# Performance work log

Measured on AMD Instinct MI355X. Metric: run time of the kernel, lower is better.

Reference implementation:

```python
import jax, jax.numpy as jnp
import numpy as np

DIM = 1024
HEADS = 16
EPS = 1e-5


def layer_norm(x, gamma, beta):
    mu = jnp.mean(x, axis=-1, keepdims=True)
    var = jnp.mean(jnp.square(x - mu), axis=-1, keepdims=True)
    return (x - mu) * jax.lax.rsqrt(var + EPS) * gamma + beta


def setup_inputs() -> dict:
    key = jax.random.key(0)
    ks = jax.random.split(key, 9)
    B, Nq, Nk = 8, 1024, 1024
    s = 1.0 / np.sqrt(DIM)
    return {
        "x": jax.random.normal(ks[0], (B, Nq, DIM), jnp.float32),
        "context": jax.random.normal(ks[1], (B, Nk, DIM), jnp.float32),
        "relative_position_bias": jax.random.normal(ks[2], (HEADS, Nq, Nk), jnp.float32),
        "Wq": jax.random.normal(ks[3], (DIM, DIM), jnp.float32) * s,
        "Wk": jax.random.normal(ks[4], (DIM, DIM), jnp.float32) * s,
        "Wv": jax.random.normal(ks[5], (DIM, DIM), jnp.float32) * s,
        "Wo": jax.random.normal(ks[6], (DIM, DIM), jnp.float32) * s,
        "bo": jnp.zeros((DIM,), jnp.float32),
        "gamma": jnp.ones((DIM,), jnp.float32),
        "beta": jnp.zeros((DIM,), jnp.float32),
    }


def reference(x, context, relative_position_bias, Wq, Wk, Wv, Wo, bo, gamma, beta):
    h = HEADS
    d = DIM // h
    scale = d ** -0.5
    xn = layer_norm(x, gamma, beta)
    cn = layer_norm(context, gamma, beta)
    B, Nq, _ = x.shape
    Nk = context.shape[1]
    # b n (h d) -> b h n d
    q = (xn @ Wq).reshape(B, Nq, h, d).transpose(0, 2, 1, 3)
    k = (cn @ Wk).reshape(B, Nk, h, d).transpose(0, 2, 1, 3)
    v = (cn @ Wv).reshape(B, Nk, h, d).transpose(0, 2, 1, 3)
    scores = jnp.einsum('bhid,bhjd->bhij', q, k) * scale
    scores = scores + relative_position_bias[None]
    attn = jax.nn.softmax(scores, axis=-1)
    out = jnp.einsum('bhij,bhjd->bhid', attn, v)
    out = out.transpose(0, 2, 1, 3).reshape(B, Nq, h * d)
    return out @ Wo + bo
```

## Files before the change

### kernel.cpp

```cpp
#include <hip/hip_runtime.h>
#include <hip/hip_bf16.h>
#include <stdint.h>

#define DIM   1024
#define HEADS 16
#define HD    64
#define NB    8
#define NTOK  1024
#define MROWS (NB*NTOK)

#define LOG2E 1.4426950408889634f
#define SCL   (0.125f * LOG2E)

typedef __attribute__((ext_vector_type(8))) _Float16 f16x8;
typedef __attribute__((ext_vector_type(4))) _Float16 f16x4;
typedef __attribute__((ext_vector_type(4))) float    f32x4;

typedef unsigned int uint_as1 __attribute__((address_space(1)));
typedef unsigned int uint_as3 __attribute__((address_space(3)));

__device__ __forceinline__ void gload16(const void* g, void* l) {
    __builtin_amdgcn_global_load_lds((const uint_as1*)g, (uint_as3*)l, 16, 0, 0);
}

__device__ __forceinline__ unsigned pkrtz(float a, float b) {
    auto h = __builtin_amdgcn_cvt_pkrtz(a, b);
    return __builtin_bit_cast(unsigned, h);
}

#if __has_builtin(__builtin_amdgcn_permlane32_swap)
__device__ __forceinline__ void swap32(unsigned& a, unsigned& b) {
    auto r = __builtin_amdgcn_permlane32_swap(a, b, false, false);
    a = r[0]; b = r[1];
}
#else
__device__ __forceinline__ void swap32(unsigned& a, unsigned& b) {
    unsigned as = (unsigned)__shfl_xor((int)a, 32, 64);
    unsigned bs = (unsigned)__shfl_xor((int)b, 32, 64);
    bool lo = ((threadIdx.x & 63) < 32);
    unsigned na = lo ? a : bs, nb = lo ? as : b;
    a = na; b = nb;
}
#endif
#if __has_builtin(__builtin_amdgcn_permlane16_swap)
__device__ __forceinline__ void swap16(unsigned& a, unsigned& b) {
    auto r = __builtin_amdgcn_permlane16_swap(a, b, false, false);
    a = r[0]; b = r[1];
}
#else
__device__ __forceinline__ void swap16(unsigned& a, unsigned& b) {
    unsigned as = (unsigned)__shfl_xor((int)a, 16, 64);
    unsigned bs = (unsigned)__shfl_xor((int)b, 16, 64);
    bool ev = ((threadIdx.x & 16) == 0);
    unsigned na = ev ? a : bs, nb = ev ? as : b;
    a = na; b = nb;
}
#endif
__device__ __forceinline__ float redmax32(float x) {
    unsigned a = __builtin_bit_cast(unsigned, x), b = a;
    swap32(a, b);
    return fmaxf(__builtin_bit_cast(float, a), __builtin_bit_cast(float, b));
}
__device__ __forceinline__ float redmax16(float x) {
    unsigned a = __builtin_bit_cast(unsigned, x), b = a;
    swap16(a, b);
    return fmaxf(__builtin_bit_cast(float, a), __builtin_bit_cast(float, b));
}
__device__ __forceinline__ float redsum32(float x) {
    unsigned a = __builtin_bit_cast(unsigned, x), b = a;
    swap32(a, b);
    return __builtin_bit_cast(float, a) + __builtin_bit_cast(float, b);
}
__device__ __forceinline__ float redsum16(float x) {
    unsigned a = __builtin_bit_cast(unsigned, x), b = a;
    swap16(a, b);
    return __builtin_bit_cast(float, a) + __builtin_bit_cast(float, b);
}

__global__ __launch_bounds__(256) void ln_kernel(const float* __restrict__ x,
                                                 const float* __restrict__ ctx,
                                                 const float* __restrict__ gamma,
                                                 const float* __restrict__ beta,
                                                 _Float16* __restrict__ xn,
                                                 _Float16* __restrict__ cn) {
    int row = blockIdx.x;
    const float* src; _Float16* dst;
    if (row < MROWS) { src = x + (size_t)row * DIM;          dst = xn + (size_t)row * DIM; }
    else             { int r = row - MROWS;
                       src = ctx + (size_t)r * DIM;          dst = cn + (size_t)r * DIM; }
    int t = threadIdx.x;
    float4 v = *(const float4*)(src + t * 4);
    float s  = v.x + v.y + v.z + v.w;
    float s2 = v.x*v.x + v.y*v.y + v.z*v.z + v.w*v.w;
    #pragma unroll
    for (int o = 32; o; o >>= 1) { s += __shfl_xor(s, o, 64); s2 += __shfl_xor(s2, o, 64); }
    __shared__ float red[8];
    int w = t >> 6, l = t & 63;
    if (l == 0) { red[w] = s; red[4 + w] = s2; }
    __syncthreads();
    s  = red[0] + red[1] + red[2] + red[3];
    s2 = red[4] + red[5] + red[6] + red[7];
    float mu   = s * (1.0f / DIM);
    float rstd = rsqrtf(s2 * (1.0f / DIM) - mu * mu + 1e-5f);
    float4 g  = *(const float4*)(gamma + t * 4);
    float4 bb = *(const float4*)(beta  + t * 4);
    f16x4 o;
    o[0] = (_Float16)((v.x - mu) * rstd * g.x + bb.x);
    o[1] = (_Float16)((v.y - mu) * rstd * g.y + bb.y);
    o[2] = (_Float16)((v.z - mu) * rstd * g.z + bb.z);
    o[3] = (_Float16)((v.w - mu) * rstd * g.w + bb.w);
    *(f16x4*)(dst + t * 4) = o;
}

__global__ __launch_bounds__(256) void biasconv_kernel(const float* __restrict__ bias,
                                                       _Float16* __restrict__ bias2) {
    size_t i = ((size_t)blockIdx.x * 256 + threadIdx.x) * 8;
    float4 a = *(const float4*)(bias + i);
    float4 b = *(const float4*)(bias + i + 4);
    f16x8 o;
    o[0] = (_Float16)(a.x * LOG2E); o[1] = (_Float16)(a.y * LOG2E);
    o[2] = (_Float16)(a.z * LOG2E); o[3] = (_Float16)(a.w * LOG2E);
    o[4] = (_Float16)(b.x * LOG2E); o[5] = (_Float16)(b.y * LOG2E);
    o[6] = (_Float16)(b.z * LOG2E); o[7] = (_Float16)(b.w * LOG2E);
    *(f16x8*)(bias2 + i) = o;
}

__global__ __launch_bounds__(256) void wtrans_kernel(const float* __restrict__ Wq, const float* __restrict__ Wk,
                                                     const float* __restrict__ Wv, const float* __restrict__ Wo,
                                                     _Float16* __restrict__ Tq, _Float16* __restrict__ Tk,
                                                     _Float16* __restrict__ Tv, _Float16* __restrict__ To) {
    __shared__ float tile[32][33];
    int m = blockIdx.z;
    const float* W = (m == 0) ? Wq : (m == 1) ? Wk : (m == 2) ? Wv : Wo;
    _Float16*    T = (m == 0) ? Tq : (m == 1) ? Tk : (m == 2) ? Tv : To;
    int j0 = blockIdx.x * 32, k0 = blockIdx.y * 32;
    int tx = threadIdx.x, ty = threadIdx.y;
    #pragma unroll
    for (int i = 0; i < 4; i++) tile[ty + i*8][tx] = W[(size_t)(k0 + ty + i*8) * DIM + j0 + tx];
    __syncthreads();
    #pragma unroll
    for (int i = 0; i < 4; i++) T[(size_t)(j0 + ty + i*8) * DIM + k0 + tx] = (_Float16)tile[tx][ty + i*8];
}

template<int MODE>
__global__ __launch_bounds__(256) void gemm_bt(const _Float16* __restrict__ A,
                                               const _Float16* __restrict__ BT,
                                               void* __restrict__ Cout,
                                               const float* __restrict__ bias) {
    __shared__ _Float16 As[128 * 32];
    __shared__ _Float16 Bs[128 * 32];
    const int K = DIM;
    int m0 = blockIdx.x * 128, n0 = blockIdx.y * 128;
    int t = threadIdx.x, w = t >> 6, l = t & 63;
    int wr = w >> 1, wc = w & 1, ln = l & 15, qtr = l >> 4;
    f32x4 acc[4][4] = {};
    int srow = t >> 2, scol = (t & 3) * 8;
    const _Float16* Ag = A  + (size_t)(m0 + srow) * K + scol;
    const _Float16* Bg = BT + (size_t)(n0 + srow) * K + scol;
    _Float16* Al = &As[(w * 16) * 32];
    _Float16* Bl = &Bs[(w * 16) * 32];
    for (int kt = 0; kt < K; kt += 32) {
        gload16(Ag,                    Al);
        gload16(Ag + (size_t)64 * K,   Al + 64 * 32);
        gload16(Bg,                    Bl);
        gload16(Bg + (size_t)64 * K,   Bl + 64 * 32);
        Ag += 32; Bg += 32;
        __syncthreads();
        f16x8 af[4], bfr[4];
        #pragma unroll
        for (int r = 0; r < 4; r++) af[r]  = *(const f16x8*)&As[(wr * 64 + r * 16 + ln) * 32 + qtr * 8];
        #pragma unroll
        for (int c = 0; c < 4; c++) bfr[c] = *(const f16x8*)&Bs[(wc * 64 + c * 16 + ln) * 32 + qtr * 8];
        #pragma unroll
        for (int r = 0; r < 4; r++)
            #pragma unroll
            for (int c = 0; c < 4; c++)
                acc[r][c] = __builtin_amdgcn_mfma_f32_16x16x32_f16(af[r], bfr[c], acc[r][c], 0, 0, 0);
        __syncthreads();
    }
    #pragma unroll
    for (int r = 0; r < 4; r++)
        #pragma unroll
        for (int c = 0; c < 4; c++) {
            int gn = n0 + wc * 64 + c * 16 + ln;
            #pragma unroll
            for (int q = 0; q < 4; q++) {
                int gm = m0 + wr * 64 + r * 16 + qtr * 4 + q;
                float v = acc[r][c][q];
                if constexpr (MODE == 0) {
                    int b = gm >> 10, n = gm & 1023, h = gn >> 6, d = gn & 63;
                    ((_Float16*)Cout)[(((size_t)(b * HEADS + h) * NTOK + n) << 6) + d] = (_Float16)v;
                } else if constexpr (MODE == 2) {
                    int b = gm >> 10, n = gm & 1023, h = gn >> 6, d = gn & 63;
                    ((_Float16*)Cout)[(((size_t)(b * HEADS + h) * HD + d) << 10) + n] = (_Float16)v;
                } else {
                    ((float*)Cout)[(size_t)gm * DIM + gn] = v + bias[gn];
                }
            }
        }
}

__global__ __launch_bounds__(256) void attn_kernel(const _Float16* __restrict__ qb,
                                                   const _Float16* __restrict__ kb,
                                                   const _Float16* __restrict__ vt,
                                                   const _Float16* __restrict__ bias2,
                                                   _Float16* __restrict__ ao) {
    __shared__ _Float16 Kt[2][64 * 64];
    __shared__ _Float16 Vs[2][64 * 64];
    int bid = blockIdx.x;
    int id2 = (bid & 7) * 128 + (bid >> 3);
    int qt = id2 & 7, h = (id2 >> 3) & 15, b = id2 >> 7;
    int q0 = qt * 128;
    int t = threadIdx.x, w = t >> 6, l = t & 63, ln = l & 15, qtr = l >> 4;
    const _Float16* qbase = qb + (size_t)(b * HEADS + h) * NTOK * HD;
    const _Float16* kbase = kb + (size_t)(b * HEADS + h) * NTOK * HD;
    const _Float16* vbase = vt + (size_t)(b * HEADS + h) * HD * NTOK;
    const _Float16* bbase = bias2 + ((size_t)h * NTOK + q0 + w * 32) * NTOK;

    f16x8 qfr[2][2];
    #pragma unroll
    for (int qf = 0; qf < 2; qf++)
        #pragma unroll
        for (int ks = 0; ks < 2; ks++)
            qfr[qf][ks] = *(const f16x8*)&qbase[(size_t)(q0 + w*32 + qf*16 + ln) * HD + ks*32 + qtr*8];

#define STAGE(BUF, J0) do {                                                     \
        int rb_ = w * 16;                                                       \
        _Float16* kl_ = &Kt[BUF][rb_ * 64];                                     \
        _Float16* vl_ = &Vs[BUF][rb_ * 64];                                     \
        int r_ = rb_ + (l >> 3); int cg_ = (l & 7) ^ (r_ & 7);                  \
        gload16(kbase + (size_t)((J0) + r_) * HD + cg_ * 8, kl_);               \
        gload16(vbase + (size_t)r_ * NTOK + (J0) + cg_ * 8, vl_);               \
        r_ += 8; cg_ = (l & 7) ^ (r_ & 7);                                      \
        gload16(kbase + (size_t)((J0) + r_) * HD + cg_ * 8, kl_ + 8 * 64);      \
        gload16(vbase + (size_t)r_ * NTOK + (J0) + cg_ * 8, vl_ + 8 * 64);      \
    } while (0)

#define LOADB(DST, TT) do {                                                     \
        _Pragma("unroll")                                                       \
        for (int qf_ = 0; qf_ < 2; qf_++)                                       \
            _Pragma("unroll")                                                   \
            for (int r_ = 0; r_ < 4; r_++)                                      \
                DST[qf_][r_] = *(const f16x4*)&bbase[(size_t)(qf_*16 + ln) * NTOK \
                                                     + (TT)*64 + qtr*4 + r_*16]; \
    } while (0)

    STAGE(0, 0);
    f16x4 bpp[2][2][4];
    LOADB(bpp[0], 0);
    __syncthreads();

    float m_run[2] = {-3.0e38f, -3.0e38f};
    float l_run[2] = {0.f, 0.f};
    f32x4 acc[2][4] = {};

    #pragma unroll 2
    for (int tt = 0; tt < 16; tt++) {
        int cur = tt & 1;
        if (tt < 15) { STAGE(cur ^ 1, (tt + 1) * 64); LOADB(bpp[cur ^ 1], tt + 1); }

        f32x4 st2[2][4] = {};
        __builtin_amdgcn_s_setprio(1);
        #pragma unroll
        for (int r = 0; r < 4; r++) {
            int row = r * 16 + ln;
            #pragma unroll
            for (int ks = 0; ks < 2; ks++) {
                f16x8 kf = *(const f16x8*)&Kt[cur][row * 64 + (((qtr + ks*4) ^ (ln & 7)) * 8)];
                st2[0][r] = __builtin_amdgcn_mfma_f32_16x16x32_f16(kf, qfr[0][ks], st2[0][r], 0, 0, 0);
                st2[1][r] = __builtin_amdgcn_mfma_f32_16x16x32_f16(kf, qfr[1][ks], st2[1][r], 0, 0, 0);
            }
        }
        __builtin_amdgcn_s_setprio(0);

        f16x8 pfr[2][2];
        #pragma unroll
        for (int qf = 0; qf < 2; qf++) {
            float sv[4][4];
            float pmax = -3.0e38f;
            #pragma unroll
            for (int r = 0; r < 4; r++) {
                f16x4 bb = bpp[cur][qf][r];
                float s0 = fmaf(st2[qf][r][0], SCL, (float)bb[0]);
                float s1 = fmaf(st2[qf][r][1], SCL, (float)bb[1]);
                float s2 = fmaf(st2[qf][r][2], SCL, (float)bb[2]);
                float s3 = fmaf(st2[qf][r][3], SCL, (float)bb[3]);
                sv[r][0] = s0; sv[r][1] = s1; sv[r][2] = s2; sv[r][3] = s3;
                pmax = fmaxf(pmax, fmaxf(fmaxf(s0, s1), fmaxf(s2, s3)));
            }
            if (!__all(pmax <= m_run[qf] + 8.f)) {
                float pm = redmax16(redmax32(pmax));
                float mnew = fmaxf(m_run[qf], pm);
                float f = exp2f(m_run[qf] - mnew);
                m_run[qf] = mnew;
                l_run[qf] *= f;
                float fm[4];
                #pragma unroll
                for (int m = 0; m < 4; m++) fm[m] = __shfl(f, (l & 48) | (qtr * 4 + m), 64);
                #pragma unroll
                for (int dg = 0; dg < 4; dg++)
                    #pragma unroll
                    for (int m = 0; m < 4; m++) acc[qf][dg][m] *= fm[m];
            }
            float sig = 0.f;
            unsigned pk2[4][2];
            #pragma unroll
            for (int r = 0; r < 4; r++) {
                float p0 = exp2f(sv[r][0] - m_run[qf]);
                float p1 = exp2f(sv[r][1] - m_run[qf]);
                float p2 = exp2f(sv[r][2] - m_run[qf]);
                float p3 = exp2f(sv[r][3] - m_run[qf]);
                sig += (p0 + p1) + (p2 + p3);
                pk2[r][0] = pkrtz(p0, p1);
                pk2[r][1] = pkrtz(p2, p3);
            }
            l_run[qf] += redsum16(redsum32(sig));

            #pragma unroll
            for (int ks = 0; ks < 2; ks++) {
                unsigned pw[4];
                #pragma unroll
                for (int c = 0; c < 2; c++) {
                    unsigned U = pk2[2*ks][c], T = pk2[2*ks + 1][c];
                    swap32(U, T);
                    swap16(U, T);
                    pw[c]     = U;
                    pw[2 + c] = T;
                }
                pfr[qf][ks] = __builtin_bit_cast(f16x8, *(const uint4*)pw);
            }
        }

        __builtin_amdgcn_s_setprio(1);
        #pragma unroll
        for (int dg = 0; dg < 4; dg++) {
            int row = dg * 16 + ln;
            #pragma unroll
            for (int ks = 0; ks < 2; ks++) {
                f16x8 vf = *(const f16x8*)&Vs[cur][row * 64 + (((qtr + ks*4) ^ (ln & 7)) * 8)];
                acc[0][dg] = __builtin_amdgcn_mfma_f32_16x16x32_f16(pfr[0][ks], vf, acc[0][dg], 0, 0, 0);
                acc[1][dg] = __builtin_amdgcn_mfma_f32_16x16x32_f16(pfr[1][ks], vf, acc[1][dg], 0, 0, 0);
            }
        }
        __builtin_amdgcn_s_setprio(0);
        __syncthreads();
    }

    #pragma unroll
    for (int qf = 0; qf < 2; qf++) {
        float inv = 1.0f / l_run[qf];
        float invm[4];
        #pragma unroll
        for (int m = 0; m < 4; m++) invm[m] = __shfl(inv, (l & 48) | (qtr * 4 + m), 64);
        size_t rowb = (size_t)b * NTOK + q0 + w * 32 + qf * 16 + qtr * 4;
        #pragma unroll
        for (int dg = 0; dg < 4; dg++)
            #pragma unroll
            for (int m = 0; m < 4; m++)
                ao[(rowb + m) * DIM + h * HD + dg * 16 + ln] = (_Float16)(acc[qf][dg][m] * invm[m]);
    }
#undef STAGE
#undef LOADB
}

extern "C" void kernel_launch(void* const* d_in, const int* in_sizes, int n_in,
                              void* d_out, int out_size, void* d_ws, size_t ws_size,
                              hipStream_t stream) {
    const float* x     = (const float*)d_in[0];
    const float* ctx   = (const float*)d_in[1];
    const float* bias  = (const float*)d_in[2];
    const float* Wq    = (const float*)d_in[3];
    const float* Wk    = (const float*)d_in[4];
    const float* Wv    = (const float*)d_in[5];
    const float* Wo    = (const float*)d_in[6];
    const float* bo    = (const float*)d_in[7];
    const float* gamma = (const float*)d_in[8];
    const float* beta  = (const float*)d_in[9];
    float* out = (float*)d_out;

    _Float16* ws  = (_Float16*)d_ws;
    _Float16* xn  = ws;
    _Float16* cn  = xn  + (size_t)MROWS * DIM;
    _Float16* wqT = cn  + (size_t)MROWS * DIM;
    _Float16* wkT = wqT + (size_t)DIM * DIM;
    _Float16* wvT = wkT + (size_t)DIM * DIM;
    _Float16* woT = wvT + (size_t)DIM * DIM;
    _Float16* qbf = woT + (size_t)DIM * DIM;
    _Float16* kbf = qbf + (size_t)MROWS * DIM;
    _Float16* vtb = kbf + (size_t)MROWS * DIM;
    _Float16* aob = vtb + (size_t)MROWS * DIM;
    _Float16* bias2 = ws;

    ln_kernel<<<dim3(2 * MROWS), dim3(256), 0, stream>>>(x, ctx, gamma, beta, xn, cn);
    wtrans_kernel<<<dim3(32, 32, 4), dim3(32, 8), 0, stream>>>(Wq, Wk, Wv, Wo, wqT, wkT, wvT, woT);
    gemm_bt<0><<<dim3(64, 8), dim3(256), 0, stream>>>(xn, wqT, qbf, nullptr);
    gemm_bt<0><<<dim3(64, 8), dim3(256), 0, stream>>>(cn, wkT, kbf, nullptr);
    gemm_bt<2><<<dim3(64, 8), dim3(256), 0, stream>>>(cn, wvT, vtb, nullptr);
    biasconv_kernel<<<dim3(8192), dim3(256), 0, stream>>>(bias, bias2);
    attn_kernel<<<dim3(NB * HEADS * 8), dim3(256), 0, stream>>>(qbf, kbf, vtb, bias2, aob);
    gemm_bt<3><<<dim3(64, 8), dim3(256), 0, stream>>>(aob, woT, out, bo);
}
```

Before: 248.4 us.

## Deepen GEMM K-tile with swizzled LDS, fold score scale into Q, reorder attention blocks

The GEMM now stages 64-wide K tiles with an XOR-swizzled LDS layout, which halves the number of barriers per K pass and avoids bank conflicts on fragment reads. The softmax scale (including log2e) is applied once in the Q projection epilogue. The attention MFMA accumulators are initialized with the position bias, which removes the per-element FMA before the max and exp. The attention block-to-(b,h,qtile) mapping is also reordered to change L2 reuse of the bias and K/V. The cost is twice the LDS per GEMM block and extra fp16 rounding of Q after scaling.

```diff
diff --git a/kernel.cpp b/kernel.cpp
--- a/kernel.cpp
+++ b/kernel.cpp
@@ -147,35 +147,40 @@
                                                const _Float16* __restrict__ BT,
                                                void* __restrict__ Cout,
                                                const float* __restrict__ bias) {
-    __shared__ _Float16 As[128 * 32];
-    __shared__ _Float16 Bs[128 * 32];
+    __shared__ _Float16 As[128 * 64];
+    __shared__ _Float16 Bs[128 * 64];
     const int K = DIM;
     int m0 = blockIdx.x * 128, n0 = blockIdx.y * 128;
     int t = threadIdx.x, w = t >> 6, l = t & 63;
     int wr = w >> 1, wc = w & 1, ln = l & 15, qtr = l >> 4;
     f32x4 acc[4][4] = {};
-    int srow = t >> 2, scol = (t & 3) * 8;
-    const _Float16* Ag = A  + (size_t)(m0 + srow) * K + scol;
-    const _Float16* Bg = BT + (size_t)(n0 + srow) * K + scol;
-    _Float16* Al = &As[(w * 16) * 32];
-    _Float16* Bl = &Bs[(w * 16) * 32];
-    for (int kt = 0; kt < K; kt += 32) {
-        gload16(Ag,                    Al);
-        gload16(Ag + (size_t)64 * K,   Al + 64 * 32);
-        gload16(Bg,                    Bl);
-        gload16(Bg + (size_t)64 * K,   Bl + 64 * 32);
-        Ag += 32; Bg += 32;
+    int srow = w * 8 + (l >> 3);
+    int cg   = (l & 7) ^ (srow & 7);
+    const _Float16* Ag = A  + (size_t)(m0 + srow) * K + cg * 8;
+    const _Float16* Bg = BT + (size_t)(n0 + srow) * K + cg * 8;
+    for (int kt = 0; kt < K; kt += 64) {
+        #pragma unroll
+        for (int p = 0; p < 4; p++) {
+            gload16(Ag + (size_t)(p * 32) * K, &As[(p * 32 + w * 8) * 64]);
+            gload16(Bg + (size_t)(p * 32) * K, &Bs[(p * 32 + w * 8) * 64]);
+        }
+        Ag += 64; Bg += 64;
         __syncthreads();
-        f16x8 af[4], bfr[4];
-        #pragma unroll
-        for (int r = 0; r < 4; r++) af[r]  = *(const f16x8*)&As[(wr * 64 + r * 16 + ln) * 32 + qtr * 8];
-        #pragma unroll
-        for (int c = 0; c < 4; c++) bfr[c] = *(const f16x8*)&Bs[(wc * 64 + c * 16 + ln) * 32 + qtr * 8];
-        #pragma unroll
-        for (int r = 0; r < 4; r++)
+        #pragma unroll
+        for (int kk = 0; kk < 2; kk++) {
+            f16x8 af[4], bfr[4];
+            #pragma unroll
+            for (int r = 0; r < 4; r++)
+                af[r]  = *(const f16x8*)&As[(wr * 64 + r * 16 + ln) * 64 + (((qtr + kk*4) ^ (ln & 7)) * 8)];
             #pragma unroll
             for (int c = 0; c < 4; c++)
-                acc[r][c] = __builtin_amdgcn_mfma_f32_16x16x32_f16(af[r], bfr[c], acc[r][c], 0, 0, 0);
+                bfr[c] = *(const f16x8*)&Bs[(wc * 64 + c * 16 + ln) * 64 + (((qtr + kk*4) ^ (ln & 7)) * 8)];
+            #pragma unroll
+            for (int r = 0; r < 4; r++)
+                #pragma unroll
+                for (int c = 0; c < 4; c++)
+                    acc[r][c] = __builtin_amdgcn_mfma_f32_16x16x32_f16(af[r], bfr[c], acc[r][c], 0, 0, 0);
+        }
         __syncthreads();
     }
     #pragma unroll
@@ -187,9 +192,10 @@
             for (int q = 0; q < 4; q++) {
                 int gm = m0 + wr * 64 + r * 16 + qtr * 4 + q;
                 float v = acc[r][c][q];
-                if constexpr (MODE == 0) {
+                if constexpr (MODE == 0 || MODE == 1) {
                     int b = gm >> 10, n = gm & 1023, h = gn >> 6, d = gn & 63;
-                    ((_Float16*)Cout)[(((size_t)(b * HEADS + h) * NTOK + n) << 6) + d] = (_Float16)v;
+                    float sc = (MODE == 1) ? SCL : 1.0f;
+                    ((_Float16*)Cout)[(((size_t)(b * HEADS + h) * NTOK + n) << 6) + d] = (_Float16)(v * sc);
                 } else if constexpr (MODE == 2) {
                     int b = gm >> 10, n = gm & 1023, h = gn >> 6, d = gn & 63;
                     ((_Float16*)Cout)[(((size_t)(b * HEADS + h) * HD + d) << 10) + n] = (_Float16)v;
@@ -208,8 +214,10 @@
     __shared__ _Float16 Kt[2][64 * 64];
     __shared__ _Float16 Vs[2][64 * 64];
     int bid = blockIdx.x;
-    int id2 = (bid & 7) * 128 + (bid >> 3);
-    int qt = id2 & 7, h = (id2 >> 3) & 15, b = id2 >> 7;
+    int rem = bid >> 3;
+    int h = (bid & 7) * 2 + (rem & 1);
+    int b = (rem >> 1) & 7;
+    int qt = rem >> 4;
     int q0 = qt * 128;
     int t = threadIdx.x, w = t >> 6, l = t & 63, ln = l & 15, qtr = l >> 4;
     const _Float16* qbase = qb + (size_t)(b * HEADS + h) * NTOK * HD;
@@ -259,7 +267,15 @@
         int cur = tt & 1;
         if (tt < 15) { STAGE(cur ^ 1, (tt + 1) * 64); LOADB(bpp[cur ^ 1], tt + 1); }
 
-        f32x4 st2[2][4] = {};
+        f32x4 st2[2][4];
+        #pragma unroll
+        for (int qf = 0; qf < 2; qf++)
+            #pragma unroll
+            for (int r = 0; r < 4; r++) {
+                f16x4 bb = bpp[cur][qf][r];
+                f32x4 ci = {(float)bb[0], (float)bb[1], (float)bb[2], (float)bb[3]};
+                st2[qf][r] = ci;
+            }
         __builtin_amdgcn_s_setprio(1);
         #pragma unroll
         for (int r = 0; r < 4; r++) {
@@ -276,18 +292,11 @@
         f16x8 pfr[2][2];
         #pragma unroll
         for (int qf = 0; qf < 2; qf++) {
-            float sv[4][4];
             float pmax = -3.0e38f;
             #pragma unroll
-            for (int r = 0; r < 4; r++) {
-                f16x4 bb = bpp[cur][qf][r];
-                float s0 = fmaf(st2[qf][r][0], SCL, (float)bb[0]);
-                float s1 = fmaf(st2[qf][r][1], SCL, (float)bb[1]);
-                float s2 = fmaf(st2[qf][r][2], SCL, (float)bb[2]);
-                float s3 = fmaf(st2[qf][r][3], SCL, (float)bb[3]);
-                sv[r][0] = s0; sv[r][1] = s1; sv[r][2] = s2; sv[r][3] = s3;
-                pmax = fmaxf(pmax, fmaxf(fmaxf(s0, s1), fmaxf(s2, s3)));
-            }
+            for (int r = 0; r < 4; r++)
+                pmax = fmaxf(pmax, fmaxf(fmaxf(st2[qf][r][0], st2[qf][r][1]),
+                                         fmaxf(st2[qf][r][2], st2[qf][r][3])));
             if (!__all(pmax <= m_run[qf] + 8.f)) {
                 float pm = redmax16(redmax32(pmax));
                 float mnew = fmaxf(m_run[qf], pm);
@@ -306,10 +315,10 @@
             unsigned pk2[4][2];
             #pragma unroll
             for (int r = 0; r < 4; r++) {
-                float p0 = exp2f(sv[r][0] - m_run[qf]);
-                float p1 = exp2f(sv[r][1] - m_run[qf]);
-                float p2 = exp2f(sv[r][2] - m_run[qf]);
-                float p3 = exp2f(sv[r][3] - m_run[qf]);
+                float p0 = exp2f(st2[qf][r][0] - m_run[qf]);
+                float p1 = exp2f(st2[qf][r][1] - m_run[qf]);
+                float p2 = exp2f(st2[qf][r][2] - m_run[qf]);
+                float p3 = exp2f(st2[qf][r][3] - m_run[qf]);
                 sig += (p0 + p1) + (p2 + p3);
                 pk2[r][0] = pkrtz(p0, p1);
                 pk2[r][1] = pkrtz(p2, p3);
@@ -393,7 +402,7 @@
 
     ln_kernel<<<dim3(2 * MROWS), dim3(256), 0, stream>>>(x, ctx, gamma, beta, xn, cn);
     wtrans_kernel<<<dim3(32, 32, 4), dim3(32, 8), 0, stream>>>(Wq, Wk, Wv, Wo, wqT, wkT, wvT, woT);
-    gemm_bt<0><<<dim3(64, 8), dim3(256), 0, stream>>>(xn, wqT, qbf, nullptr);
+    gemm_bt<1><<<dim3(64, 8), dim3(256), 0, stream>>>(xn, wqT, qbf, nullptr);
     gemm_bt<0><<<dim3(64, 8), dim3(256), 0, stream>>>(cn, wkT, kbf, nullptr);
     gemm_bt<2><<<dim3(64, 8), dim3(256), 0, stream>>>(cn, wvT, vtb, nullptr);
     biasconv_kernel<<<dim3(8192), dim3(256), 0, stream>>>(bias, bias2);
```

New measurement: 232.3 us. -6.5%, faster.
